# Kernel tuning notes

Hardware: AMD Instinct MI355X
Metric: run time of the kernel (lower is better)

## Reference

```python
import jax, jax.numpy as jnp
import numpy as np

# cfg.SIAMESE constants (typical FastVOD values)
ROIS_PER_IMAGE = 128
FG_PER_IMAGE = 32          # round(0.25 * 128)
FG_THRESH = 0.7
BG_THRESH_HI = 0.3
BG_THRESH_LO = 0.0

B, N, G = 16, 65536, 64


def _make_boxes(key, shape, img=1000.0):
    k1, k2, k3, k4 = jax.random.split(key, 4)
    x1 = jax.random.uniform(k1, shape) * (img - 64.0)
    y1 = jax.random.uniform(k2, shape) * (img - 64.0)
    w = jax.random.uniform(k3, shape) * 200.0 + 8.0
    h = jax.random.uniform(k4, shape) * 200.0 + 8.0
    return jnp.stack([x1, y1, jnp.minimum(x1 + w, img), jnp.minimum(y1 + h, img)], axis=-1)


def setup_inputs() -> dict:
    key = jax.random.key(0)
    kr, kg, kl, kt, kp, kf, kb, km = jax.random.split(key, 8)
    roi_boxes = _make_boxes(kr, (B, N))                      # [B,N,4]
    all_rois = jnp.concatenate([jnp.zeros((B, N, 1)), roi_boxes], axis=-1)  # [B,N,5]
    gtb = _make_boxes(kg, (B, G))                            # [B,G,4]
    labels = jax.random.randint(kl, (B, G), 1, 31).astype(jnp.float32)
    tids = jax.random.randint(kt, (B, G), 0, 1000).astype(jnp.float32)
    # pad last 8 gt per image with zero boxes (common padding pattern)
    pad = jnp.arange(G) >= G - 8
    gtb = jnp.where(pad[None, :, None], 0.0, gtb)
    labels = jnp.where(pad[None, :], 0.0, labels)
    gt_boxes = jnp.concatenate([gtb, labels[..., None], tids[..., None]], axis=-1)  # [B,G,6]
    u_perm = jax.random.uniform(kp, (B, N + G))
    u_fg = jax.random.uniform(kf, (B, ROIS_PER_IMAGE))
    u_bg = jax.random.uniform(kb, (B, ROIS_PER_IMAGE))
    return {"all_rois": all_rois, "gt_boxes": gt_boxes, "u_perm": u_perm,
            "u_fg": u_fg, "u_bg": u_bg}


def _bbox_overlaps_batch(rois, gt):
    # rois: [B,Nt,5] (idx,x1,y1,x2,y2), gt: [B,G,4]
    a = rois[:, :, 1:5]
    aw = a[:, :, 2] - a[:, :, 0] + 1.0
    ah = a[:, :, 3] - a[:, :, 1] + 1.0
    gw = gt[:, :, 2] - gt[:, :, 0] + 1.0
    gh = gt[:, :, 3] - gt[:, :, 1] + 1.0
    area_a = aw * ah                                  # [B,Nt]
    area_g = gw * gh                                  # [B,G]
    iw = jnp.clip(jnp.minimum(a[:, :, None, 2], gt[:, None, :, 2])
                  - jnp.maximum(a[:, :, None, 0], gt[:, None, :, 0]) + 1.0, 0.0)
    ih = jnp.clip(jnp.minimum(a[:, :, None, 3], gt[:, None, :, 3])
                  - jnp.maximum(a[:, :, None, 1], gt[:, None, :, 1]) + 1.0, 0.0)
    inter = iw * ih                                   # [B,Nt,G]
    ov = inter / (area_a[:, :, None] + area_g[:, None, :] - inter)
    gt_zero = (gw == 1.0) & (gh == 1.0)
    a_zero = (aw == 1.0) & (ah == 1.0)
    ov = jnp.where(gt_zero[:, None, :], 0.0, ov)
    ov = jnp.where(a_zero[:, :, None], -1.0, ov)
    return ov


def _sample_one(max_ov, up, uf, ub):
    # max_ov: [Nt]; replicates the per-image fg/bg sampling loop, vectorized.
    R = ROIS_PER_IMAGE
    fg_mask = max_ov >= FG_THRESH
    bg_mask = ((max_ov < BG_THRESH_HI) & (max_ov >= BG_THRESH_LO)) | (max_ov < 0)
    fg_num = fg_mask.sum()
    bg_num = bg_mask.sum()
    # randomly-ordered fg (resp. bg) indices come first after the argsort
    fg_order = jnp.argsort(jnp.where(fg_mask, up, 2.0))
    bg_order = jnp.argsort(jnp.where(bg_mask, up, 2.0))
    both = (fg_num > 0) & (bg_num > 0)
    only_fg = (fg_num > 0) & (bg_num == 0)
    fg_this = jnp.where(both, jnp.minimum(FG_PER_IMAGE, fg_num),
                        jnp.where(only_fg, R, 0))
    pos = jnp.arange(R)
    # fg: permutation (no replacement) when both present, else uniform w/ replacement
    fg_repl = jnp.clip((uf * fg_num).astype(jnp.int32), 0, jnp.maximum(fg_num - 1, 0))
    fg_pick = jnp.where(only_fg, fg_order[fg_repl], fg_order[pos])
    # bg: always uniform with replacement
    bg_repl = jnp.clip((ub * bg_num).astype(jnp.int32), 0, jnp.maximum(bg_num - 1, 0))
    bg_pick = bg_order[bg_repl]
    is_fg = pos < fg_this
    keep = jnp.where(is_fg, fg_pick, bg_pick)
    return keep, is_fg


def reference(all_rois, gt_boxes, u_perm, u_fg, u_bg):
    # append gt boxes as proposals: [B, N+G, 5]
    gt_append = jnp.concatenate(
        [jnp.zeros_like(gt_boxes[:, :, :1]), gt_boxes[:, :, :4]], axis=-1)
    rois_all = jnp.concatenate([all_rois, gt_append], axis=1)
    ov = _bbox_overlaps_batch(rois_all, gt_boxes[:, :, :4])      # [B,Nt,G]
    max_ov = jnp.max(ov, axis=2)
    gt_assign = jnp.argmax(ov, axis=2)                            # [B,Nt]
    labels = jnp.take_along_axis(gt_boxes[:, :, 4], gt_assign, axis=1)   # [B,Nt]
    tids = jnp.take_along_axis(gt_boxes[:, :, 5], gt_assign, axis=1)
    keep, is_fg = jax.vmap(_sample_one)(max_ov, u_perm, u_fg, u_bg)      # [B,R]
    lab_b = jnp.where(is_fg, jnp.take_along_axis(labels, keep, axis=1), 0.0)
    tid_b = jnp.where(is_fg, jnp.take_along_axis(tids, keep, axis=1), -1.0)
    rois_b = jnp.take_along_axis(rois_all, keep[:, :, None], axis=1)     # [B,R,5]
    batch_idx = jnp.arange(rois_b.shape[0], dtype=rois_b.dtype)[:, None]
    rois_b = rois_b.at[:, :, 0].set(jnp.broadcast_to(batch_idx, rois_b.shape[:2]))
    return rois_b, lab_b, tid_b
```

## Files before the change

kernel.cpp:

```cpp
#include <hip/hip_runtime.h>

#define B_   16
#define N_   65536
#define G_   64
#define M_   (N_ + G_)
#define R_   128
#define FGP  32
#define NB_  16384
#define NCH_ 32
#define CHUNK_ (NB_ / NCH_)
#define NROW_ 32
#define FW_  (NB_ / 32)
#define TPB_  256

__global__ void prep_kernel(const float* __restrict__ gt_boxes,
                            int*    __restrict__ zbase,
                            float4* __restrict__ gt4,
                            float*  __restrict__ garea,
                            int*    __restrict__ jmax)
{
    const int gid = blockIdx.x * blockDim.x + threadIdx.x;
    const int total = NROW_ * NB_ + NROW_ * FW_;
    for (int idx = gid; idx < total; idx += gridDim.x * blockDim.x) zbase[idx] = 0;
    if (gid < B_ * G_) {
        int b = gid >> 6, j = gid & 63;
        const float* g = gt_boxes + gid * 6;
        float x1 = g[0], y1 = g[1], x2 = g[2], y2 = g[3];
        float gw = x2 - x1 + 1.0f, gh = y2 - y1 + 1.0f;
        bool gz = (gw == 1.0f) && (gh == 1.0f);
        gt4[gid] = gz ? make_float4(3.0e8f, 3.0e8f, -3.0e8f, -3.0e8f)
                      : make_float4(x1, y1, x2, y2);
        garea[gid] = gw * gh;
        unsigned long long alive = __ballot(!gz);
        if (j == 0) { int last = 63 - __clzll(alive); jmax[b] = (last + 8) & ~7; }
    }
}

__global__ void iou_kernel(const float* __restrict__ all_rois,
                           const float* __restrict__ gt_boxes,
                           const float4* __restrict__ gt4,
                           const float*  __restrict__ garea,
                           const int*    __restrict__ jmax,
                           const float*  __restrict__ u_perm,
                           unsigned*     __restrict__ packed,
                           int*          __restrict__ hist)
{
    __shared__ float4 sg[G_];
    __shared__ float  sa[G_];
    const int b   = blockIdx.y;
    const int tid = threadIdx.x;
    if (tid < G_) { sg[tid] = gt4[b * G_ + tid]; sa[tid] = garea[b * G_ + tid]; }
    __syncthreads();

    const int i = blockIdx.x * blockDim.x + tid;
    if (i >= M_) return;

    float x1, y1, x2, y2;
    if (i < N_) {
        const float* p = all_rois + ((size_t)b * N_ + i) * 5;
        x1 = p[1]; y1 = p[2]; x2 = p[3]; y2 = p[4];
    } else {
        const float* p = gt_boxes + (b * G_ + (i - N_)) * 6;
        x1 = p[0]; y1 = p[1]; x2 = p[2]; y2 = p[3];
    }
    float aw = x2 - x1 + 1.0f, ah = y2 - y1 + 1.0f;
    float area_a = aw * ah;
    bool  a_zero = (aw == 1.0f) && (ah == 1.0f);

    const int jm = jmax[b];
    float ib = 0.0f, ub = 1.0f;
    for (int jj = 0; jj < jm; jj += 8) {
        #pragma unroll
        for (int kk = 0; kk < 8; ++kk) {
            const int j = jj + kk;
            const float4 g  = sg[j];
            const float  ga = sa[j];
            float iw  = fmaxf(fminf(x2, g.z) - fmaxf(x1, g.x) + 1.0f, 0.0f);
            float ih2 = fmaxf(fminf(y2, g.w) - fmaxf(y1, g.y) + 1.0f, 0.0f);
            float inter = iw * ih2;
            float uni   = area_a + ga - inter;
            float hi1 = inter * ub, lo1 = fmaf(inter, ub, -hi1);
            float hi2 = ib * uni,   lo2 = fmaf(ib, uni, -hi2);
            bool gt = (hi1 > hi2) || ((hi1 == hi2) && (lo1 > lo2));
            if (gt) { ib = inter; ub = uni; }
        }
    }
    float best = ib / ub;
    if (a_zero) best = -1.0f;

    bool fg = best >= 0.7f;
    bool bg = best < 0.3f;
    unsigned pk = 0xFFFFFFFFu;
    if (fg || bg) {
        int cls = fg ? 0 : 1;
        float u = u_perm[(size_t)b * M_ + i];
        int bucket = min(max((int)(u * (float)NB_), 0), NB_ - 1);
        pk = ((unsigned)cls << 16) | (unsigned)bucket;
        atomicAdd(&hist[(size_t)(b * 2 + cls) * NB_ + bucket], 1);
    }
    packed[(size_t)b * M_ + i] = pk;
}

__global__ __launch_bounds__(512) void scanflag_kernel(
    int*      __restrict__ hist,
    unsigned* __restrict__ flags,
    int*      __restrict__ cnt_g,
    const float* __restrict__ u_fg,
    const float* __restrict__ u_bg,
    int4*     __restrict__ pick)
{
    __shared__ int scoarse[2][NCH_];
    __shared__ int scnt[2];
    __shared__ int swt[2][8], swb[2][8];
    const int bb  = blockIdx.x;
    const int tid = threadIdx.x;
    const int lane = tid & 63, w = tid >> 6;

    for (int rr = 0; rr < 2; ++rr) {
        const int row = bb * 2 + rr;
        int4* h4 = (int4*)(hist + (size_t)row * NB_ + tid * 32);
        int v[32];
        #pragma unroll
        for (int q = 0; q < 8; ++q) {
            int4 x4 = h4[q];
            v[q*4] = x4.x; v[q*4+1] = x4.y; v[q*4+2] = x4.z; v[q*4+3] = x4.w;
        }
        int run = 0;
        #pragma unroll
        for (int q = 0; q < 32; ++q) { int x = v[q]; v[q] = run; run += x; }
        int x = run;
        #pragma unroll
        for (int d = 1; d < 64; d <<= 1) {
            int y = __shfl_up(x, d);
            if (lane >= d) x += y;
        }
        if (lane == 63) swt[rr][w] = x;
        __syncthreads();
        if (tid == 0) {
            int a = 0;
            #pragma unroll
            for (int q = 0; q < 8; ++q) { swb[rr][q] = a; a += swt[rr][q]; }
        }
        __syncthreads();
        const int incl  = swb[rr][w] + x;
        const int texcl = incl - run;
        #pragma unroll
        for (int q = 0; q < 8; ++q) {
            h4[q] = make_int4(v[q*4] + texcl, v[q*4+1] + texcl,
                              v[q*4+2] + texcl, v[q*4+3] + texcl);
        }
        if ((tid & 15) == 15) scoarse[rr][tid >> 4] = incl;
        if (tid == 511) { scnt[rr] = incl; cnt_g[row] = incl; }
    }
    __syncthreads();

    if (tid < R_) {
        const int pos = tid;
        const int fgn = scnt[0], bgn = scnt[1];
        const bool both    = (fgn > 0) && (bgn > 0);
        const bool only_fg = (fgn > 0) && (bgn == 0);
        const int fg_this  = both ? min(FGP, fgn) : (only_fg ? R_ : 0);
        const bool is_fg   = pos < fg_this;
        int cls, rank, cnum;
        if (is_fg) {
            cls = 0; cnum = fgn;
            if (only_fg) {
                float uf = u_fg[bb * R_ + pos];
                int kk = (int)(uf * (float)fgn);
                rank = min(max(kk, 0), max(fgn - 1, 0));
            } else {
                rank = pos;
            }
        } else {
            cls = 1; cnum = bgn;
            float ubv = u_bg[bb * R_ + pos];
            int kk = (int)(ubv * (float)bgn);
            rank = min(max(kk, 0), max(bgn - 1, 0));
        }
        int4 p4 = make_int4(0, 0, 0, is_fg ? 1 : 0);
        if (cnum > 0) {
            const int row = bb * 2 + cls;
            const int* sce = scoarse[cls];
            int c = 0;
            while (c < NCH_ - 1 && sce[c] <= rank) ++c;
            const int* Er = hist + (size_t)row * NB_;
            int lo = c * CHUNK_, hi = c * CHUNK_ + CHUNK_ - 1;
            while (lo < hi) {
                int mid = (lo + hi + 1) >> 1;
                if (Er[mid] <= rank) lo = mid; else hi = mid - 1;
            }
            const int start = Er[lo];
            const int next  = (lo < NB_ - 1) ? Er[lo + 1] : cnum;
            atomicOr(&flags[row * FW_ + (lo >> 5)], 1u << (lo & 31));
            p4 = make_int4(start, next - start, rank - start, is_fg ? 1 : 0);
        }
        pick[bb * R_ + pos] = p4;
    }
}

__global__ void scatter_kernel(const unsigned* __restrict__ packed,
                               const unsigned* __restrict__ flags,
                               int*            __restrict__ E,
                               int*            __restrict__ buckets)
{
    const int b = blockIdx.y;
    const int i = blockIdx.x * blockDim.x + threadIdx.x;
    if (i >= M_) return;
    unsigned pk = packed[(size_t)b * M_ + i];
    if (pk == 0xFFFFFFFFu) return;
    const int cls = (int)(pk >> 16);
    const int bucket = (int)(pk & 0xFFFFu);
    const int row = b * 2 + cls;
    unsigned w = flags[row * FW_ + (bucket >> 5)];
    if (!(w & (1u << (bucket & 31)))) return;
    int p = atomicAdd(&E[(size_t)row * NB_ + bucket], 1);
    buckets[(size_t)row * M_ + p] = i;
}

__global__ void sample_kernel(const float* __restrict__ all_rois,
                              const float* __restrict__ gt_boxes,
                              const float4* __restrict__ gt4,
                              const float*  __restrict__ garea,
                              const float* __restrict__ u_perm,
                              const int*  __restrict__ cnt,
                              const int4* __restrict__ pick,
                              const int*  __restrict__ buckets,
                              float*      __restrict__ out)
{
    const int b   = blockIdx.x;
    const int pos = threadIdx.x;
    const int4 pk = pick[b * R_ + pos];
    const bool is_fg = pk.w != 0;
    const int  cls   = is_fg ? 0 : 1;

    int keep = 0;
    if (pk.y > 0) {
        const int row = b * 2 + cls;
        const int*   be = buckets + (size_t)row * M_ + pk.x;
        const float* up = u_perm + (size_t)b * M_;
        const int cnt2 = pk.y, r = pk.z;
        for (int t2 = 0; t2 < cnt2; ++t2) {
            int it = be[t2]; float ut = up[it];
            int rk = 0;
            for (int s2 = 0; s2 < cnt2; ++s2) {
                if (s2 == t2) continue;
                int is2 = be[s2]; float us = up[is2];
                if (us < ut || (us == ut && is2 < it)) rk++;
            }
            if (rk == r) { keep = it; break; }
        }
    }

    float ox1, oy1, ox2, oy2;
    if (keep < N_) {
        const float* p = all_rois + ((size_t)b * N_ + keep) * 5;
        ox1 = p[1]; oy1 = p[2]; ox2 = p[3]; oy2 = p[4];
    } else {
        const float* p = gt_boxes + (b * G_ + (keep - N_)) * 6;
        ox1 = p[0]; oy1 = p[1]; ox2 = p[2]; oy2 = p[3];
    }
    float* ro = out + ((size_t)b * R_ + pos) * 5;
    ro[0] = (float)b; ro[1] = ox1; ro[2] = oy1; ro[3] = ox2; ro[4] = oy2;

    float lab = 0.0f, tidv = -1.0f;
    if (is_fg) {
        float aw = ox2 - ox1 + 1.0f, ah = oy2 - oy1 + 1.0f;
        float area_a = aw * ah;
        float bestv = -1e30f;
        int   bi    = 0;
        for (int j = 0; j < G_; ++j) {
            const float4 g  = gt4[b * G_ + j];
            const float  ga = garea[b * G_ + j];
            float iw  = fmaxf(fminf(ox2, g.z) - fmaxf(ox1, g.x) + 1.0f, 0.0f);
            float ih2 = fmaxf(fminf(oy2, g.w) - fmaxf(oy1, g.y) + 1.0f, 0.0f);
            float inter = iw * ih2;
            float ov = inter / (area_a + ga - inter);
            if (ov > bestv) { bestv = ov; bi = j; }
        }
        lab  = gt_boxes[(b * G_ + bi) * 6 + 4];
        tidv = gt_boxes[(b * G_ + bi) * 6 + 5];
    }
    out[(size_t)B_ * R_ * 5 + b * R_ + pos] = lab;
    out[(size_t)B_ * R_ * 5 + (size_t)B_ * R_ + b * R_ + pos] = tidv;
}

extern "C" void kernel_launch(void* const* d_in, const int* in_sizes, int n_in,
                              void* d_out, int out_size, void* d_ws, size_t ws_size,
                              hipStream_t stream)
{
    const float* all_rois = (const float*)d_in[0];
    const float* gt_boxes = (const float*)d_in[1];
    const float* u_perm   = (const float*)d_in[2];
    const float* u_fg     = (const float*)d_in[3];
    const float* u_bg     = (const float*)d_in[4];
    float* out = (float*)d_out;

    int*      hist    = (int*)d_ws;
    unsigned* flags   = (unsigned*)(hist + (size_t)NROW_ * NB_);
    int*      cnt     = (int*)(flags + NROW_ * FW_);
    int4*     pick    = (int4*)(cnt + 32);
    unsigned* packed  = (unsigned*)(pick + B_ * R_);
    int*      buckets = (int*)(packed + (size_t)B_ * M_);
    float4*   gt4     = (float4*)(buckets + (size_t)NROW_ * M_);
    float*    garea   = (float*)(gt4 + B_ * G_);
    int*      jmax    = (int*)(garea + B_ * G_);

    prep_kernel<<<512, TPB_, 0, stream>>>(gt_boxes, hist, gt4, garea, jmax);

    dim3 grid1((M_ + TPB_ - 1) / TPB_, B_);
    iou_kernel<<<grid1, TPB_, 0, stream>>>(all_rois, gt_boxes, gt4, garea, jmax,
                                           u_perm, packed, hist);
    scanflag_kernel<<<B_, 512, 0, stream>>>(hist, flags, cnt, u_fg, u_bg, pick);
    scatter_kernel<<<grid1, TPB_, 0, stream>>>(packed, flags, hist, buckets);
    sample_kernel<<<B_, R_, 0, stream>>>(all_rois, gt_boxes, gt4, garea, u_perm,
                                         cnt, pick, buckets, out);
}
```

Measured before the change: 97.11 us.

## Shrink histogram, parallelize scan over both classes, vectorize scatter, split sampling

The bucket histogram drops from 16384 to 4096 bins. The prefix scan now runs both classes at once in a 1024-thread block, keeps the prefix in shared memory for a single binary search, and clears the flags itself instead of leaving that to prep. The IoU loop compares inter/(area sum) and computes the union only once at the end. Scatter reads four packed entries per thread, and sampling uses 32 blocks of 64 threads instead of 16 blocks of 128. Fewer bins shrink the zeroing and scan work but make the selected buckets larger, so the quadratic rank loop in sampling does more work per pick.

```diff
diff --git a/kernel.cpp b/kernel.cpp
--- a/kernel.cpp
+++ b/kernel.cpp
@@ -6,22 +6,19 @@
 #define M_   (N_ + G_)
 #define R_   128
 #define FGP  32
-#define NB_  16384
-#define NCH_ 32
-#define CHUNK_ (NB_ / NCH_)
+#define NB_  4096
 #define NROW_ 32
 #define FW_  (NB_ / 32)
 #define TPB_  256
 
 __global__ void prep_kernel(const float* __restrict__ gt_boxes,
-                            int*    __restrict__ zbase,
+                            int*    __restrict__ hist,
                             float4* __restrict__ gt4,
                             float*  __restrict__ garea,
                             int*    __restrict__ jmax)
 {
     const int gid = blockIdx.x * blockDim.x + threadIdx.x;
-    const int total = NROW_ * NB_ + NROW_ * FW_;
-    for (int idx = gid; idx < total; idx += gridDim.x * blockDim.x) zbase[idx] = 0;
+    for (int idx = gid; idx < NROW_ * NB_; idx += gridDim.x * blockDim.x) hist[idx] = 0;
     if (gid < B_ * G_) {
         int b = gid >> 6, j = gid & 63;
         const float* g = gt_boxes + gid * 6;
@@ -68,7 +65,7 @@
     bool  a_zero = (aw == 1.0f) && (ah == 1.0f);
 
     const int jm = jmax[b];
-    float ib = 0.0f, ub = 1.0f;
+    float ib = 0.0f, sb = 1.0f;
     for (int jj = 0; jj < jm; jj += 8) {
         #pragma unroll
         for (int kk = 0; kk < 8; ++kk) {
@@ -78,14 +75,14 @@
             float iw  = fmaxf(fminf(x2, g.z) - fmaxf(x1, g.x) + 1.0f, 0.0f);
             float ih2 = fmaxf(fminf(y2, g.w) - fmaxf(y1, g.y) + 1.0f, 0.0f);
             float inter = iw * ih2;
-            float uni   = area_a + ga - inter;
-            float hi1 = inter * ub, lo1 = fmaf(inter, ub, -hi1);
-            float hi2 = ib * uni,   lo2 = fmaf(ib, uni, -hi2);
+            float s     = area_a + ga;
+            float hi1 = inter * sb, lo1 = fmaf(inter, sb, -hi1);
+            float hi2 = ib * s,     lo2 = fmaf(ib, s, -hi2);
             bool gt = (hi1 > hi2) || ((hi1 == hi2) && (lo1 > lo2));
-            if (gt) { ib = inter; ub = uni; }
-        }
-    }
-    float best = ib / ub;
+            if (gt) { ib = inter; sb = s; }
+        }
+    }
+    float best = ib / (sb - ib);
     if (a_zero) best = -1.0f;
 
     bool fg = best >= 0.7f;
@@ -101,57 +98,58 @@
     packed[(size_t)b * M_ + i] = pk;
 }
 
-__global__ __launch_bounds__(512) void scanflag_kernel(
+__global__ __launch_bounds__(1024) void scanflag_kernel(
     int*      __restrict__ hist,
     unsigned* __restrict__ flags,
-    int*      __restrict__ cnt_g,
     const float* __restrict__ u_fg,
     const float* __restrict__ u_bg,
     int4*     __restrict__ pick)
 {
-    __shared__ int scoarse[2][NCH_];
+    __shared__ int spfx[2][NB_];
+    __shared__ int swt[2][8], swb[2][8];
     __shared__ int scnt[2];
-    __shared__ int swt[2][8], swb[2][8];
     const int bb  = blockIdx.x;
     const int tid = threadIdx.x;
-    const int lane = tid & 63, w = tid >> 6;
-
-    for (int rr = 0; rr < 2; ++rr) {
-        const int row = bb * 2 + rr;
-        int4* h4 = (int4*)(hist + (size_t)row * NB_ + tid * 32);
-        int v[32];
+    const int rr  = tid >> 9;
+    const int t   = tid & 511;
+    const int lane = tid & 63, w = (tid >> 6) & 7;
+
+    if (tid < 2 * FW_) flags[bb * 2 * FW_ + tid] = 0;
+
+    const int row = bb * 2 + rr;
+    int* h = hist + (size_t)row * NB_ + t * 8;
+    int4* h4 = (int4*)h;
+    int v[8];
+    {
+        int4 x4 = h4[0];
+        v[0] = x4.x; v[1] = x4.y; v[2] = x4.z; v[3] = x4.w;
+        x4 = h4[1];
+        v[4] = x4.x; v[5] = x4.y; v[6] = x4.z; v[7] = x4.w;
+    }
+    int run = 0;
+    #pragma unroll
+    for (int k = 0; k < 8; ++k) { int x = v[k]; v[k] = run; run += x; }
+    int x = run;
+    #pragma unroll
+    for (int d = 1; d < 64; d <<= 1) {
+        int y = __shfl_up(x, d);
+        if (lane >= d) x += y;
+    }
+    if (lane == 63) swt[rr][w] = x;
+    __syncthreads();
+    if ((tid & 511) == 0) {
+        int a = 0;
         #pragma unroll
-        for (int q = 0; q < 8; ++q) {
-            int4 x4 = h4[q];
-            v[q*4] = x4.x; v[q*4+1] = x4.y; v[q*4+2] = x4.z; v[q*4+3] = x4.w;
-        }
-        int run = 0;
-        #pragma unroll
-        for (int q = 0; q < 32; ++q) { int x = v[q]; v[q] = run; run += x; }
-        int x = run;
-        #pragma unroll
-        for (int d = 1; d < 64; d <<= 1) {
-            int y = __shfl_up(x, d);
-            if (lane >= d) x += y;
-        }
-        if (lane == 63) swt[rr][w] = x;
-        __syncthreads();
-        if (tid == 0) {
-            int a = 0;
-            #pragma unroll
-            for (int q = 0; q < 8; ++q) { swb[rr][q] = a; a += swt[rr][q]; }
-        }
-        __syncthreads();
-        const int incl  = swb[rr][w] + x;
-        const int texcl = incl - run;
-        #pragma unroll
-        for (int q = 0; q < 8; ++q) {
-            h4[q] = make_int4(v[q*4] + texcl, v[q*4+1] + texcl,
-                              v[q*4+2] + texcl, v[q*4+3] + texcl);
-        }
-        if ((tid & 15) == 15) scoarse[rr][tid >> 4] = incl;
-        if (tid == 511) { scnt[rr] = incl; cnt_g[row] = incl; }
-    }
+        for (int q = 0; q < 8; ++q) { swb[rr][q] = a; a += swt[rr][q]; }
+        scnt[rr] = a;
+    }
+    __syncthreads();
+    const int texcl = swb[rr][w] + x - run;
+    int e[8];
+    #pragma unroll
+    for (int k = 0; k < 8; ++k) { e[k] = texcl + v[k]; spfx[rr][t * 8 + k] = e[k]; }
+    h4[0] = make_int4(e[0], e[1], e[2], e[3]);
+    h4[1] = make_int4(e[4], e[5], e[6], e[7]);
     __syncthreads();
 
     if (tid < R_) {
@@ -179,19 +177,15 @@
         }
         int4 p4 = make_int4(0, 0, 0, is_fg ? 1 : 0);
         if (cnum > 0) {
-            const int row = bb * 2 + cls;
-            const int* sce = scoarse[cls];
-            int c = 0;
-            while (c < NCH_ - 1 && sce[c] <= rank) ++c;
-            const int* Er = hist + (size_t)row * NB_;
-            int lo = c * CHUNK_, hi = c * CHUNK_ + CHUNK_ - 1;
+            const int* P = spfx[cls];
+            int lo = 0, hi = NB_ - 1;
             while (lo < hi) {
                 int mid = (lo + hi + 1) >> 1;
-                if (Er[mid] <= rank) lo = mid; else hi = mid - 1;
+                if (P[mid] <= rank) lo = mid; else hi = mid - 1;
             }
-            const int start = Er[lo];
-            const int next  = (lo < NB_ - 1) ? Er[lo + 1] : cnum;
-            atomicOr(&flags[row * FW_ + (lo >> 5)], 1u << (lo & 31));
+            const int start = P[lo];
+            const int next  = (lo < NB_ - 1) ? P[lo + 1] : cnum;
+            atomicOr(&flags[(bb * 2 + cls) * FW_ + (lo >> 5)], 1u << (lo & 31));
             p4 = make_int4(start, next - start, rank - start, is_fg ? 1 : 0);
         }
         pick[bb * R_ + pos] = p4;
@@ -203,18 +197,23 @@
                                int*            __restrict__ E,
                                int*            __restrict__ buckets)
 {
-    const int b = blockIdx.y;
-    const int i = blockIdx.x * blockDim.x + threadIdx.x;
-    if (i >= M_) return;
-    unsigned pk = packed[(size_t)b * M_ + i];
-    if (pk == 0xFFFFFFFFu) return;
-    const int cls = (int)(pk >> 16);
-    const int bucket = (int)(pk & 0xFFFFu);
-    const int row = b * 2 + cls;
-    unsigned w = flags[row * FW_ + (bucket >> 5)];
-    if (!(w & (1u << (bucket & 31)))) return;
-    int p = atomicAdd(&E[(size_t)row * NB_ + bucket], 1);
-    buckets[(size_t)row * M_ + p] = i;
+    const int b  = blockIdx.y;
+    const int i4 = blockIdx.x * blockDim.x + threadIdx.x;
+    if (i4 >= M_ / 4) return;
+    const uint4 p = ((const uint4*)(packed + (size_t)b * M_))[i4];
+    const unsigned pks[4] = { p.x, p.y, p.z, p.w };
+    #pragma unroll
+    for (int k = 0; k < 4; ++k) {
+        unsigned pk = pks[k];
+        if (pk == 0xFFFFFFFFu) continue;
+        const int cls = (int)(pk >> 16);
+        const int bucket = (int)(pk & 0xFFFFu);
+        const int row = b * 2 + cls;
+        unsigned w = flags[row * FW_ + (bucket >> 5)];
+        if (!(w & (1u << (bucket & 31)))) continue;
+        int pp = atomicAdd(&E[(size_t)row * NB_ + bucket], 1);
+        buckets[(size_t)row * M_ + pp] = i4 * 4 + k;
+    }
 }
 
 __global__ void sample_kernel(const float* __restrict__ all_rois,
@@ -222,13 +221,12 @@
                               const float4* __restrict__ gt4,
                               const float*  __restrict__ garea,
                               const float* __restrict__ u_perm,
-                              const int*  __restrict__ cnt,
                               const int4* __restrict__ pick,
                               const int*  __restrict__ buckets,
                               float*      __restrict__ out)
 {
-    const int b   = blockIdx.x;
-    const int pos = threadIdx.x;
+    const int b   = blockIdx.x >> 1;
+    const int pos = ((blockIdx.x & 1) << 6) | threadIdx.x;
     const int4 pk = pick[b * R_ + pos];
     const bool is_fg = pk.w != 0;
     const int  cls   = is_fg ? 0 : 1;
@@ -297,21 +295,22 @@
 
     int*      hist    = (int*)d_ws;
     unsigned* flags   = (unsigned*)(hist + (size_t)NROW_ * NB_);
-    int*      cnt     = (int*)(flags + NROW_ * FW_);
-    int4*     pick    = (int4*)(cnt + 32);
+    int4*     pick    = (int4*)(flags + NROW_ * FW_);
     unsigned* packed  = (unsigned*)(pick + B_ * R_);
     int*      buckets = (int*)(packed + (size_t)B_ * M_);
     float4*   gt4     = (float4*)(buckets + (size_t)NROW_ * M_);
     float*    garea   = (float*)(gt4 + B_ * G_);
     int*      jmax    = (int*)(garea + B_ * G_);
 
-    prep_kernel<<<512, TPB_, 0, stream>>>(gt_boxes, hist, gt4, garea, jmax);
+    prep_kernel<<<256, TPB_, 0, stream>>>(gt_boxes, hist, gt4, garea, jmax);
 
     dim3 grid1((M_ + TPB_ - 1) / TPB_, B_);
     iou_kernel<<<grid1, TPB_, 0, stream>>>(all_rois, gt_boxes, gt4, garea, jmax,
                                            u_perm, packed, hist);
-    scanflag_kernel<<<B_, 512, 0, stream>>>(hist, flags, cnt, u_fg, u_bg, pick);
-    scatter_kernel<<<grid1, TPB_, 0, stream>>>(packed, flags, hist, buckets);
-    sample_kernel<<<B_, R_, 0, stream>>>(all_rois, gt_boxes, gt4, garea, u_perm,
-                                         cnt, pick, buckets, out);
-}
+    scanflag_kernel<<<B_, 1024, 0, stream>>>(hist, flags, u_fg, u_bg, pick);
+
+    dim3 grid3((M_ / 4 + TPB_ - 1) / TPB_, B_);
+    scatter_kernel<<<grid3, TPB_, 0, stream>>>(packed, flags, hist, buckets);
+    sample_kernel<<<B_ * 2, 64, 0, stream>>>(all_rois, gt_boxes, gt4, garea,
+                                             u_perm, pick, buckets, out);
+}
```

Result: slower. 217.2 us (+123.6%).
